# Kernel tuning notes

Hardware: AMD Instinct MI355X
Metric: run time of the kernel (lower is better)

## Reference

```python
import jax, jax.numpy as jnp
import numpy as np

N = 100000
F_IN = 128
F_OUT = 128
NNZ = 1_600_000  # avg degree 16


def spmm(rows, cols, vals, X, n):
    """Sparse [n,n] (COO: rows, cols, vals) times dense X [n,d] -> [n,d]."""
    return jax.ops.segment_sum(vals[:, None] * X[cols], rows, num_segments=n)


def setup_inputs() -> dict:
    key = jax.random.key(0)
    ks = jax.random.split(key, 8)
    x = jax.random.normal(ks[0], (N, F_IN), dtype=jnp.float32)
    W = jax.random.normal(ks[1], (F_IN, F_OUT), dtype=jnp.float32) * 0.05
    kernel = jnp.ones((N, 1), dtype=jnp.float32)  # tf.ones_initializer
    phi0_rows = jax.random.randint(ks[2], (NNZ,), 0, N, dtype=jnp.int64)
    phi0_cols = jax.random.randint(ks[3], (NNZ,), 0, N, dtype=jnp.int64)
    phi0_vals = jax.random.uniform(ks[4], (NNZ,), dtype=jnp.float32)
    phi1_rows = jax.random.randint(ks[5], (NNZ,), 0, N, dtype=jnp.int64)
    phi1_cols = jax.random.randint(ks[6], (NNZ,), 0, N, dtype=jnp.int64)
    phi1_vals = jax.random.uniform(ks[7], (NNZ,), dtype=jnp.float32)
    return {
        "x": x, "W": W, "kernel": kernel,
        "phi0_rows": phi0_rows, "phi0_cols": phi0_cols, "phi0_vals": phi0_vals,
        "phi1_rows": phi1_rows, "phi1_cols": phi1_cols, "phi1_vals": phi1_vals,
    }


def reference(x, W, kernel, phi0_rows, phi0_cols, phi0_vals,
              phi1_rows, phi1_cols, phi1_vals):
    # X' = x @ W  (dense feature projection)
    X_prime = x @ W  # [N, F_OUT]
    # X'_t = phi0 @ X'  (SpMM with wavelet basis)
    X_t = spmm(phi0_rows, phi0_cols, phi0_vals, X_prime, N)
    # out = phi1 @ (kernel * X'_t)  (elementwise spectral scaling then SpMM)
    out = spmm(phi1_rows, phi1_cols, phi1_vals, kernel * X_t, N)
    return jax.nn.relu(out)
```

## Files before the change

### kernel.cpp

```cpp
#include <hip/hip_runtime.h>


constexpr int kN = 100000;
constexpr int kF = 128;
constexpr int kNNZ = 1600000;

constexpr int kBuckets = (kN + 255) / 256;
constexpr int kBucketCap = 4608;
constexpr int kChunk = 7168;
constexpr int kChunkBlocks = (kNNZ + kChunk - 1) / kChunk;
constexpr int kSlotsPerMat = kChunkBlocks * kChunk;
constexpr int kDirStride = kBuckets + 1;
constexpr int kTransBlocks = 64;
constexpr int kSortBlocks = 2 * kBuckets;
constexpr int kGemmBlocks = (kN + 127) / 128;
constexpr int kRowBlocks = kN * 32 / 256;

typedef short bf16x8 __attribute__((ext_vector_type(8)));
typedef float f32x4 __attribute__((ext_vector_type(4)));
typedef unsigned short ushort4v __attribute__((ext_vector_type(4)));

__device__ __forceinline__ unsigned short f32_to_bf16(float f) {
    unsigned int u = __float_as_uint(f);
    u += 0x7fffu + ((u >> 16) & 1u);
    return (unsigned short)(u >> 16);
}
__device__ __forceinline__ float bf16_to_f32(unsigned short h) {
    return __uint_as_float((unsigned int)h << 16);
}

__global__ __launch_bounds__(256) void scatter_transpose(
    const float* __restrict__ W, unsigned short* __restrict__ Wt,
    const int* __restrict__ r0, const int* __restrict__ c0, const float* __restrict__ v0,
    const int* __restrict__ r1, const int* __restrict__ c1, const float* __restrict__ v1,
    unsigned long long* __restrict__ stg, unsigned short* __restrict__ dir) {
    const int t = threadIdx.x;
    if (blockIdx.x < kTransBlocks) {
        const int e = blockIdx.x * 256 + t;
        const int n = e & 127, k = e >> 7;
        Wt[n * 128 + k] = f32_to_bf16(W[e]);
        return;
    }

    __shared__ unsigned long long recs[kChunk];
    __shared__ int hist[kDirStride];
    __shared__ int cur[kDirStride];
    __shared__ int sc2[256];

    const int b = blockIdx.x - kTransBlocks;
    const bool m1 = b >= kChunkBlocks;
    const int cb = m1 ? b - kChunkBlocks : b;
    const int* rows = m1 ? r1 : r0;
    const int* cols = m1 ? c1 : c0;
    const float* vals = m1 ? v1 : v0;
    unsigned long long* dst = stg + (size_t)b * kChunk;
    unsigned short* dirm = dir + (size_t)b * kDirStride;

    for (int i = t; i < kDirStride; i += 256) hist[i] = 0;
    __syncthreads();

    const int base0 = cb * kChunk;
    const int cnt = min(kNNZ - base0, kChunk);

    for (int j = t; j < cnt; j += 256) atomicAdd(&hist[rows[base0 + j] >> 8], 1);
    __syncthreads();

    int s = 0;
    if (t < 196) s = hist[2 * t] + hist[2 * t + 1];
    sc2[t] = (t < 196) ? s : 0;
    __syncthreads();
    #pragma unroll
    for (int off = 1; off < 256; off <<= 1) {
        const int add = (t >= off) ? sc2[t - off] : 0;
        __syncthreads();
        sc2[t] += add;
        __syncthreads();
    }
    if (t < 196) {
        const int ex = sc2[t] - s;
        cur[2 * t] = ex;
        cur[2 * t + 1] = ex + hist[2 * t];
        dirm[2 * t] = (unsigned short)ex;
        dirm[2 * t + 1] = (unsigned short)(ex + hist[2 * t]);
    }
    __syncthreads();

    for (int j = t; j < cnt; j += 256) {
        const int idx = base0 + j;
        const int r = rows[idx];
        const int bk = r >> 8;
        const int pos = atomicAdd(&cur[bk], 1);
        const unsigned int key = ((unsigned int)(r & 255) << 17) | (unsigned int)cols[idx];
        recs[pos] = ((unsigned long long)__float_as_uint(vals[idx]) << 32) | key;
    }
    __syncthreads();

    for (int j = t; j < cnt; j += 256) dst[j] = recs[j];
}

__global__ __launch_bounds__(512) void sort_gemm(
    const unsigned long long* __restrict__ stg,
    const unsigned short* __restrict__ dir,
    unsigned long long* __restrict__ sortedG,
    int* __restrict__ rs, int* __restrict__ re,
    const float* __restrict__ x, const unsigned short* __restrict__ Wt,
    unsigned short* __restrict__ Xpb) {
    __shared__ __align__(16) char smem[41728];
    const int t = threadIdx.x;

    if (blockIdx.x < kSortBlocks) {
        unsigned long long* sorted = (unsigned long long*)smem;
        int* rlen = (int*)(smem + 36864);
        int* gst  = (int*)(smem + 36864 + 896);
        int* hist = (int*)(smem + 36864 + 1792);
        int* sc   = (int*)(smem + 36864 + 2816);
        int* cur  = (int*)(smem + 36864 + 3840);

        const int bidx = blockIdx.x;
        const bool m1 = bidx >= kBuckets;
        const int bk = m1 ? bidx - kBuckets : bidx;
        const unsigned long long* stgm = stg + (m1 ? (size_t)kSlotsPerMat : 0);

        if (t < kChunkBlocks) {
            const unsigned short* dd =
                dir + (size_t)((m1 ? kChunkBlocks : 0) + t) * kDirStride;
            const int s = dd[bk];
            rlen[t] = dd[bk + 1] - s;
            gst[t] = t * kChunk + s;
        }
        if (t < 256) hist[t] = 0;
        __syncthreads();

        const int g = t >> 5;
        const int lane = t & 31;

        for (int blk = g; blk < kChunkBlocks; blk += 16) {
            const int len = rlen[blk];
            const int gs = gst[blk];
            for (int i = lane; i < len; i += 32) {
                const unsigned int lo = (unsigned int)stgm[gs + i];
                atomicAdd(&hist[(lo >> 17) & 255], 1);
            }
        }
        __syncthreads();

        const int v = (t < 256) ? hist[t] : 0;
        if (t < 256) sc[t] = v;
        __syncthreads();
        #pragma unroll
        for (int off = 1; off < 256; off <<= 1) {
            const int add = (t < 256 && t >= off) ? sc[t - off] : 0;
            __syncthreads();
            if (t < 256) sc[t] += add;
            __syncthreads();
        }
        if (t < 256) cur[t] = sc[t] - v;
        __syncthreads();

        for (int blk = g; blk < kChunkBlocks; blk += 16) {
            const int len = rlen[blk];
            const int gs = gst[blk];
            for (int i = lane; i < len; i += 32) {
                const unsigned long long p = stgm[gs + i];
                const int lrow = (int)(((unsigned int)p >> 17) & 255);
                sorted[atomicAdd(&cur[lrow], 1)] = p;
            }
        }
        __syncthreads();

        const int nrec = sc[255];
        const size_t outBase = (size_t)bidx * kBucketCap;
        for (int j = t; j < nrec; j += 512) sortedG[outBase + j] = sorted[j];
        if (t < 256) {
            const int row = bk * 256 + t;
            if (row < kN) {
                const int rg = (m1 ? kN : 0) + row;
                rs[rg] = (int)outBase + sc[t] - hist[t];
                re[rg] = (int)outBase + sc[t];
            }
        }
    } else {
        unsigned short* xs = (unsigned short*)smem;
        const int rowBase = (blockIdx.x - kSortBlocks) * 128;

        {
            const int lrow = t >> 2;
            const int q = t & 3;
            int srow = rowBase + lrow;
            if (srow >= kN) srow = kN - 1;
            const float4* xr = (const float4*)(x + (size_t)srow * kF) + q * 8;
            #pragma unroll
            for (int i = 0; i < 8; ++i) {
                const float4 f = xr[i];
                ushort4v h;
                h.x = f32_to_bf16(f.x); h.y = f32_to_bf16(f.y);
                h.z = f32_to_bf16(f.z); h.w = f32_to_bf16(f.w);
                const int kidx = q * 32 + i * 4;
                *(ushort4v*)&xs[lrow * 128 + (kidx ^ ((lrow & 7) << 3))] = h;
            }
        }
        __syncthreads();

        const int w = t >> 6;
        const int l = t & 63;
        const int lr = l & 15;
        const int lq = l >> 4;

        f32x4 acc[8];
        #pragma unroll
        for (int n = 0; n < 8; ++n) acc[n] = (f32x4){0.f, 0.f, 0.f, 0.f};

        const int arow = w * 16 + lr;
        #pragma unroll
        for (int ks = 0; ks < 4; ++ks) {
            const int akidx = ks * 32 + lq * 8;
            const bf16x8 a = *(const bf16x8*)&xs[arow * 128 + (akidx ^ ((arow & 7) << 3))];
            #pragma unroll
            for (int n = 0; n < 8; ++n) {
                const int bn = n * 16 + lr;
                const bf16x8 b = *(const bf16x8*)(Wt + bn * 128 + akidx);
                acc[n] = __builtin_amdgcn_mfma_f32_16x16x32_bf16(a, b, acc[n], 0, 0, 0);
            }
        }

        #pragma unroll
        for (int j = 0; j < 4; ++j) {
            const int row = rowBase + w * 16 + lq * 4 + j;
            if (row < kN) {
                unsigned short* orow = Xpb + (size_t)row * kF + lr;
                #pragma unroll
                for (int n = 0; n < 8; ++n) orow[n * 16] = f32_to_bf16(acc[n][j]);
            }
        }
    }
}

template <bool ROW_SCALE, bool RELU, bool OUT_BF16>
__global__ __launch_bounds__(256) void spmm_csr(const int* __restrict__ rs,
                                                const int* __restrict__ re,
                                                const unsigned long long* __restrict__ rec,
                                                const float* __restrict__ scale,
                                                const unsigned short* __restrict__ Xin,
                                                void* __restrict__ Xout) {
    const int tid = blockIdx.x * 256 + threadIdx.x;
    const int r = tid >> 5;
    const int lane = tid & 31;

    const int s = rs[r];
    const int e = re[r];

    float4 acc = make_float4(0.f, 0.f, 0.f, 0.f);

    for (int base = s; base < e; base += 32) {
        int cl = 0;
        float vl = 0.f;
        if (base + lane < e) {
            const unsigned long long p = __builtin_nontemporal_load(&rec[base + lane]);
            cl = (int)((unsigned int)p & 0x1FFFF);
            vl = __uint_as_float((unsigned int)(p >> 32));
        }
        const int m4 = (min(32, e - base) + 3) & ~3;
        for (int j = 0; j < m4; j += 4) {
            const int c0 = __shfl(cl, j, 32);
            const int c1 = __shfl(cl, j + 1, 32);
            const int c2 = __shfl(cl, j + 2, 32);
            const int c3 = __shfl(cl, j + 3, 32);
            const float w0 = __shfl(vl, j, 32);
            const float w1 = __shfl(vl, j + 1, 32);
            const float w2 = __shfl(vl, j + 2, 32);
            const float w3 = __shfl(vl, j + 3, 32);
            const ushort4v x0 = *(const ushort4v*)(Xin + (size_t)c0 * kF + lane * 4);
            const ushort4v x1 = *(const ushort4v*)(Xin + (size_t)c1 * kF + lane * 4);
            const ushort4v x2 = *(const ushort4v*)(Xin + (size_t)c2 * kF + lane * 4);
            const ushort4v x3 = *(const ushort4v*)(Xin + (size_t)c3 * kF + lane * 4);
            acc.x = fmaf(w0, bf16_to_f32(x0.x), acc.x);
            acc.y = fmaf(w0, bf16_to_f32(x0.y), acc.y);
            acc.z = fmaf(w0, bf16_to_f32(x0.z), acc.z);
            acc.w = fmaf(w0, bf16_to_f32(x0.w), acc.w);
            acc.x = fmaf(w1, bf16_to_f32(x1.x), acc.x);
            acc.y = fmaf(w1, bf16_to_f32(x1.y), acc.y);
            acc.z = fmaf(w1, bf16_to_f32(x1.z), acc.z);
            acc.w = fmaf(w1, bf16_to_f32(x1.w), acc.w);
            acc.x = fmaf(w2, bf16_to_f32(x2.x), acc.x);
            acc.y = fmaf(w2, bf16_to_f32(x2.y), acc.y);
            acc.z = fmaf(w2, bf16_to_f32(x2.z), acc.z);
            acc.w = fmaf(w2, bf16_to_f32(x2.w), acc.w);
            acc.x = fmaf(w3, bf16_to_f32(x3.x), acc.x);
            acc.y = fmaf(w3, bf16_to_f32(x3.y), acc.y);
            acc.z = fmaf(w3, bf16_to_f32(x3.z), acc.z);
            acc.w = fmaf(w3, bf16_to_f32(x3.w), acc.w);
        }
    }
    if (ROW_SCALE) {
        const float k = scale[r];
        acc.x *= k; acc.y *= k; acc.z *= k; acc.w *= k;
    }
    if (RELU) {
        acc.x = fmaxf(acc.x, 0.f); acc.y = fmaxf(acc.y, 0.f);
        acc.z = fmaxf(acc.z, 0.f); acc.w = fmaxf(acc.w, 0.f);
    }
    if (OUT_BF16) {
        ushort4v o;
        o.x = f32_to_bf16(acc.x); o.y = f32_to_bf16(acc.y);
        o.z = f32_to_bf16(acc.z); o.w = f32_to_bf16(acc.w);
        __builtin_nontemporal_store(
            o, (ushort4v*)((unsigned short*)Xout + (size_t)r * kF + lane * 4));
    } else {
        f32x4 o;
        o.x = acc.x; o.y = acc.y; o.z = acc.z; o.w = acc.w;
        __builtin_nontemporal_store(o, (f32x4*)Xout + (size_t)r * 32 + lane);
    }
}

extern "C" void kernel_launch(void* const* d_in, const int* in_sizes, int n_in,
                              void* d_out, int out_size, void* d_ws, size_t ws_size,
                              hipStream_t stream) {
    const float* x    = (const float*)d_in[0];
    const float* W    = (const float*)d_in[1];
    const float* kern = (const float*)d_in[2];
    const int*   p0r  = (const int*)d_in[3];
    const int*   p0c  = (const int*)d_in[4];
    const float* p0v  = (const float*)d_in[5];
    const int*   p1r  = (const int*)d_in[6];
    const int*   p1c  = (const int*)d_in[7];
    const float* p1v  = (const float*)d_in[8];

    unsigned long long* stg = (unsigned long long*)d_out;

    char* w = (char*)d_ws;
    size_t off = 0;
    unsigned short* Xpb = (unsigned short*)(w + off); off += (size_t)kN * kF * 2;
    unsigned short* Xtb = (unsigned short*)(w + off); off += (size_t)kN * kF * 2;
    unsigned short* Wt = (unsigned short*)(w + off);  off += 128 * 128 * 2;
    unsigned short* dir = (unsigned short*)(w + off);
    off += (size_t)2 * kChunkBlocks * kDirStride * 2;
    off = (off + 15) & ~(size_t)15;
    unsigned long long* sortedG = (unsigned long long*)(w + off);
    off += (size_t)2 * kBuckets * kBucketCap * 8;
    int* rs = (int*)(w + off);                        off += (size_t)2 * kN * 4;
    int* re = (int*)(w + off);                        off += (size_t)2 * kN * 4;

    scatter_transpose<<<kTransBlocks + 2 * kChunkBlocks, 256, 0, stream>>>(
        W, Wt, p0r, p0c, p0v, p1r, p1c, p1v, stg, dir);

    sort_gemm<<<kSortBlocks + kGemmBlocks, 512, 0, stream>>>(
        stg, dir, sortedG, rs, re, x, Wt, Xpb);

    spmm_csr<true, false, true><<<kRowBlocks, 256, 0, stream>>>(
        rs, re, sortedG, kern, Xpb, Xtb);

    spmm_csr<false, true, false><<<kRowBlocks, 256, 0, stream>>>(
        rs + kN, re + kN, sortedG, nullptr, Xtb, (float*)d_out);
}
```

Measured before the change: 207.3 us.

## Co-schedule phi1 bucket sort with first SpMM in one launch

Moves the phi1 bucket sort out of the sort+GEMM kernel and into a new combined kernel that also runs the first SpMM, so sorting for the second matrix overlaps with the first sparse product. This splits the stages more evenly and shortens the critical path of the sort+GEMM launch. The first SpMM now runs with 512-thread blocks that share launch and occupancy with the heavier sort blocks, which may change scheduling balance and LDS-limited occupancy.

```diff
diff --git a/kernel.cpp b/kernel.cpp
--- a/kernel.cpp
+++ b/kernel.cpp
@@ -12,8 +12,8 @@
 constexpr int kSlotsPerMat = kChunkBlocks * kChunk;
 constexpr int kDirStride = kBuckets + 1;
 constexpr int kTransBlocks = 64;
-constexpr int kSortBlocks = 2 * kBuckets;
 constexpr int kGemmBlocks = (kN + 127) / 128;
+constexpr int kSpmmBlocks512 = kN * 32 / 512;
 constexpr int kRowBlocks = kN * 32 / 256;
 
 typedef short bf16x8 __attribute__((ext_vector_type(8)));
@@ -98,154 +98,91 @@
     for (int j = t; j < cnt; j += 256) dst[j] = recs[j];
 }
 
-__global__ __launch_bounds__(512) void sort_gemm(
+__device__ __forceinline__ void sort_bucket_body(
+    char* smem, int bk, int matSel,
     const unsigned long long* __restrict__ stg,
     const unsigned short* __restrict__ dir,
     unsigned long long* __restrict__ sortedG,
-    int* __restrict__ rs, int* __restrict__ re,
-    const float* __restrict__ x, const unsigned short* __restrict__ Wt,
-    unsigned short* __restrict__ Xpb) {
-    __shared__ __align__(16) char smem[41728];
+    int* __restrict__ rs, int* __restrict__ re) {
+    unsigned long long* sorted = (unsigned long long*)smem;
+    int* rlen = (int*)(smem + 36864);
+    int* gst  = (int*)(smem + 36864 + 896);
+    int* hist = (int*)(smem + 36864 + 1792);
+    int* sc   = (int*)(smem + 36864 + 2816);
+    int* cur  = (int*)(smem + 36864 + 3840);
+
     const int t = threadIdx.x;
-
-    if (blockIdx.x < kSortBlocks) {
-        unsigned long long* sorted = (unsigned long long*)smem;
-        int* rlen = (int*)(smem + 36864);
-        int* gst  = (int*)(smem + 36864 + 896);
-        int* hist = (int*)(smem + 36864 + 1792);
-        int* sc   = (int*)(smem + 36864 + 2816);
-        int* cur  = (int*)(smem + 36864 + 3840);
-
-        const int bidx = blockIdx.x;
-        const bool m1 = bidx >= kBuckets;
-        const int bk = m1 ? bidx - kBuckets : bidx;
-        const unsigned long long* stgm = stg + (m1 ? (size_t)kSlotsPerMat : 0);
-
-        if (t < kChunkBlocks) {
-            const unsigned short* dd =
-                dir + (size_t)((m1 ? kChunkBlocks : 0) + t) * kDirStride;
-            const int s = dd[bk];
-            rlen[t] = dd[bk + 1] - s;
-            gst[t] = t * kChunk + s;
-        }
-        if (t < 256) hist[t] = 0;
-        __syncthreads();
-
-        const int g = t >> 5;
-        const int lane = t & 31;
-
-        for (int blk = g; blk < kChunkBlocks; blk += 16) {
-            const int len = rlen[blk];
-            const int gs = gst[blk];
-            for (int i = lane; i < len; i += 32) {
-                const unsigned int lo = (unsigned int)stgm[gs + i];
-                atomicAdd(&hist[(lo >> 17) & 255], 1);
-            }
-        }
-        __syncthreads();
-
-        const int v = (t < 256) ? hist[t] : 0;
-        if (t < 256) sc[t] = v;
-        __syncthreads();
-        #pragma unroll
-        for (int off = 1; off < 256; off <<= 1) {
-            const int add = (t < 256 && t >= off) ? sc[t - off] : 0;
-            __syncthreads();
-            if (t < 256) sc[t] += add;
-            __syncthreads();
-        }
-        if (t < 256) cur[t] = sc[t] - v;
-        __syncthreads();
-
-        for (int blk = g; blk < kChunkBlocks; blk += 16) {
-            const int len = rlen[blk];
-            const int gs = gst[blk];
-            for (int i = lane; i < len; i += 32) {
-                const unsigned long long p = stgm[gs + i];
-                const int lrow = (int)(((unsigned int)p >> 17) & 255);
-                sorted[atomicAdd(&cur[lrow], 1)] = p;
-            }
-        }
-        __syncthreads();
-
-        const int nrec = sc[255];
-        const size_t outBase = (size_t)bidx * kBucketCap;
-        for (int j = t; j < nrec; j += 512) sortedG[outBase + j] = sorted[j];
-        if (t < 256) {
-            const int row = bk * 256 + t;
-            if (row < kN) {
-                const int rg = (m1 ? kN : 0) + row;
-                rs[rg] = (int)outBase + sc[t] - hist[t];
-                re[rg] = (int)outBase + sc[t];
-            }
-        }
-    } else {
-        unsigned short* xs = (unsigned short*)smem;
-        const int rowBase = (blockIdx.x - kSortBlocks) * 128;
-
-        {
-            const int lrow = t >> 2;
-            const int q = t & 3;
-            int srow = rowBase + lrow;
-            if (srow >= kN) srow = kN - 1;
-            const float4* xr = (const float4*)(x + (size_t)srow * kF) + q * 8;
-            #pragma unroll
-            for (int i = 0; i < 8; ++i) {
-                const float4 f = xr[i];
-                ushort4v h;
-                h.x = f32_to_bf16(f.x); h.y = f32_to_bf16(f.y);
-                h.z = f32_to_bf16(f.z); h.w = f32_to_bf16(f.w);
-                const int kidx = q * 32 + i * 4;
-                *(ushort4v*)&xs[lrow * 128 + (kidx ^ ((lrow & 7) << 3))] = h;
-            }
-        }
-        __syncthreads();
-
-        const int w = t >> 6;
-        const int l = t & 63;
-        const int lr = l & 15;
-        const int lq = l >> 4;
-
-        f32x4 acc[8];
-        #pragma unroll
-        for (int n = 0; n < 8; ++n) acc[n] = (f32x4){0.f, 0.f, 0.f, 0.f};
-
-        const int arow = w * 16 + lr;
-        #pragma unroll
-        for (int ks = 0; ks < 4; ++ks) {
-            const int akidx = ks * 32 + lq * 8;
-            const bf16x8 a = *(const bf16x8*)&xs[arow * 128 + (akidx ^ ((arow & 7) << 3))];
-            #pragma unroll
-            for (int n = 0; n < 8; ++n) {
-                const int bn = n * 16 + lr;
-                const bf16x8 b = *(const bf16x8*)(Wt + bn * 128 + akidx);
-                acc[n] = __builtin_amdgcn_mfma_f32_16x16x32_bf16(a, b, acc[n], 0, 0, 0);
-            }
-        }
-
-        #pragma unroll
-        for (int j = 0; j < 4; ++j) {
-            const int row = rowBase + w * 16 + lq * 4 + j;
-            if (row < kN) {
-                unsigned short* orow = Xpb + (size_t)row * kF + lr;
-                #pragma unroll
-                for (int n = 0; n < 8; ++n) orow[n * 16] = f32_to_bf16(acc[n][j]);
-            }
+    const unsigned long long* stgm = stg + (matSel ? (size_t)kSlotsPerMat : 0);
+
+    if (t < kChunkBlocks) {
+        const unsigned short* dd =
+            dir + (size_t)(matSel * kChunkBlocks + t) * kDirStride;
+        const int s = dd[bk];
+        rlen[t] = dd[bk + 1] - s;
+        gst[t] = t * kChunk + s;
+    }
+    if (t < 256) hist[t] = 0;
+    __syncthreads();
+
+    const int g = t >> 5;
+    const int lane = t & 31;
+
+    for (int blk = g; blk < kChunkBlocks; blk += 16) {
+        const int len = rlen[blk];
+        const int gs = gst[blk];
+        for (int i = lane; i < len; i += 32) {
+            const unsigned int lo = (unsigned int)stgm[gs + i];
+            atomicAdd(&hist[(lo >> 17) & 255], 1);
+        }
+    }
+    __syncthreads();
+
+    const int v = (t < 256) ? hist[t] : 0;
+    if (t < 256) sc[t] = v;
+    __syncthreads();
+    #pragma unroll
+    for (int off = 1; off < 256; off <<= 1) {
+        const int add = (t < 256 && t >= off) ? sc[t - off] : 0;
+        __syncthreads();
+        if (t < 256) sc[t] += add;
+        __syncthreads();
+    }
+    if (t < 256) cur[t] = sc[t] - v;
+    __syncthreads();
+
+    for (int blk = g; blk < kChunkBlocks; blk += 16) {
+        const int len = rlen[blk];
+        const int gs = gst[blk];
+        for (int i = lane; i < len; i += 32) {
+            const unsigned long long p = stgm[gs + i];
+            const int lrow = (int)(((unsigned int)p >> 17) & 255);
+            sorted[atomicAdd(&cur[lrow], 1)] = p;
+        }
+    }
+    __syncthreads();
+
+    const int nrec = sc[255];
+    const int bidx = matSel * kBuckets + bk;
+    const size_t outBase = (size_t)bidx * kBucketCap;
+    for (int j = t; j < nrec; j += 512) sortedG[outBase + j] = sorted[j];
+    if (t < 256) {
+        const int row = bk * 256 + t;
+        if (row < kN) {
+            const int rg = matSel * kN + row;
+            rs[rg] = (int)outBase + sc[t] - hist[t];
+            re[rg] = (int)outBase + sc[t];
         }
     }
 }
 
 template <bool ROW_SCALE, bool RELU, bool OUT_BF16>
-__global__ __launch_bounds__(256) void spmm_csr(const int* __restrict__ rs,
-                                                const int* __restrict__ re,
-                                                const unsigned long long* __restrict__ rec,
-                                                const float* __restrict__ scale,
-                                                const unsigned short* __restrict__ Xin,
-                                                void* __restrict__ Xout) {
-    const int tid = blockIdx.x * 256 + threadIdx.x;
-    const int r = tid >> 5;
-    const int lane = tid & 31;
-
+__device__ __forceinline__ void spmm_row_body(
+    int r, int lane,
+    const int* __restrict__ rs, const int* __restrict__ re,
+    const unsigned long long* __restrict__ rec,
+    const float* __restrict__ scale,
+    const unsigned short* __restrict__ Xin,
+    void* __restrict__ Xout) {
     const int s = rs[r];
     const int e = re[r];
 
@@ -312,6 +249,103 @@
     }
 }
 
+__global__ __launch_bounds__(512) void sort_gemm(
+    const unsigned long long* __restrict__ stg,
+    const unsigned short* __restrict__ dir,
+    unsigned long long* __restrict__ sortedG,
+    int* __restrict__ rs, int* __restrict__ re,
+    const float* __restrict__ x, const unsigned short* __restrict__ Wt,
+    unsigned short* __restrict__ Xpb) {
+    __shared__ __align__(16) char smem[41728];
+    const int t = threadIdx.x;
+
+    if (blockIdx.x < kBuckets) {
+        sort_bucket_body(smem, blockIdx.x, 0, stg, dir, sortedG, rs, re);
+    } else {
+        unsigned short* xs = (unsigned short*)smem;
+        const int rowBase = (blockIdx.x - kBuckets) * 128;
+
+        {
+            const int lrow = t >> 2;
+            const int q = t & 3;
+            int srow = rowBase + lrow;
+            if (srow >= kN) srow = kN - 1;
+            const float4* xr = (const float4*)(x + (size_t)srow * kF) + q * 8;
+            #pragma unroll
+            for (int i = 0; i < 8; ++i) {
+                const float4 f = xr[i];
+                ushort4v h;
+                h.x = f32_to_bf16(f.x); h.y = f32_to_bf16(f.y);
+                h.z = f32_to_bf16(f.z); h.w = f32_to_bf16(f.w);
+                const int kidx = q * 32 + i * 4;
+                *(ushort4v*)&xs[lrow * 128 + (kidx ^ ((lrow & 7) << 3))] = h;
+            }
+        }
+        __syncthreads();
+
+        const int w = t >> 6;
+        const int l = t & 63;
+        const int lr = l & 15;
+        const int lq = l >> 4;
+
+        f32x4 acc[8];
+        #pragma unroll
+        for (int n = 0; n < 8; ++n) acc[n] = (f32x4){0.f, 0.f, 0.f, 0.f};
+
+        const int arow = w * 16 + lr;
+        #pragma unroll
+        for (int ks = 0; ks < 4; ++ks) {
+            const int akidx = ks * 32 + lq * 8;
+            const bf16x8 a = *(const bf16x8*)&xs[arow * 128 + (akidx ^ ((arow & 7) << 3))];
+            #pragma unroll
+            for (int n = 0; n < 8; ++n) {
+                const int bn = n * 16 + lr;
+                const bf16x8 b = *(const bf16x8*)(Wt + bn * 128 + akidx);
+                acc[n] = __builtin_amdgcn_mfma_f32_16x16x32_bf16(a, b, acc[n], 0, 0, 0);
+            }
+        }
+
+        #pragma unroll
+        for (int j = 0; j < 4; ++j) {
+            const int row = rowBase + w * 16 + lq * 4 + j;
+            if (row < kN) {
+                unsigned short* orow = Xpb + (size_t)row * kF + lr;
+                #pragma unroll
+                for (int n = 0; n < 8; ++n) orow[n * 16] = f32_to_bf16(acc[n][j]);
+            }
+        }
+    }
+}
+
+__global__ __launch_bounds__(512) void sort_spmm(
+    const unsigned long long* __restrict__ stg,
+    const unsigned short* __restrict__ dir,
+    unsigned long long* __restrict__ sortedG,
+    int* __restrict__ rs, int* __restrict__ re,
+    const float* __restrict__ kern,
+    const unsigned short* __restrict__ Xpb,
+    unsigned short* __restrict__ Xtb) {
+    __shared__ __align__(16) char smem[41728];
+
+    if (blockIdx.x < kBuckets) {
+        sort_bucket_body(smem, blockIdx.x, 1, stg, dir, sortedG, rs, re);
+    } else {
+        const int t = threadIdx.x;
+        const int r = (blockIdx.x - kBuckets) * 16 + (t >> 5);
+        spmm_row_body<true, false, true>(r, t & 31, rs, re, sortedG, kern, Xpb, Xtb);
+    }
+}
+
+__global__ __launch_bounds__(256) void spmm_csr(const int* __restrict__ rs,
+                                                const int* __restrict__ re,
+                                                const unsigned long long* __restrict__ rec,
+                                                const unsigned short* __restrict__ Xin,
+                                                float* __restrict__ Xout) {
+    const int tid = blockIdx.x * 256 + threadIdx.x;
+    spmm_row_body<false, true, false>(tid >> 5, tid & 31, rs, re, rec, nullptr,
+                                      Xin, Xout);
+}
+
 extern "C" void kernel_launch(void* const* d_in, const int* in_sizes, int n_in,
                               void* d_out, int out_size, void* d_ws, size_t ws_size,
                               hipStream_t stream) {
@@ -343,12 +377,12 @@
     scatter_transpose<<<kTransBlocks + 2 * kChunkBlocks, 256, 0, stream>>>(
         W, Wt, p0r, p0c, p0v, p1r, p1c, p1v, stg, dir);
 
-    sort_gemm<<<kSortBlocks + kGemmBlocks, 512, 0, stream>>>(
+    sort_gemm<<<kBuckets + kGemmBlocks, 512, 0, stream>>>(
         stg, dir, sortedG, rs, re, x, Wt, Xpb);
 
-    spmm_csr<true, false, true><<<kRowBlocks, 256, 0, stream>>>(
-        rs, re, sortedG, kern, Xpb, Xtb);
-
-    spmm_csr<false, true, false><<<kRowBlocks, 256, 0, stream>>>(
-        rs + kN, re + kN, sortedG, nullptr, Xtb, (float*)d_out);
-}
+    sort_spmm<<<kBuckets + kSpmmBlocks512, 512, 0, stream>>>(
+        stg, dir, sortedG, rs, re, kern, Xpb, Xtb);
+
+    spmm_csr<<<kRowBlocks, 256, 0, stream>>>(rs + kN, re + kN, sortedG, Xtb,
+                                             (float*)d_out);
+}
```

Measured after the change: 205.4 us. About the same (-0.9%).
